# Performance work log

Hardware: AMD Instinct MI355X
Metric: run time of the kernel (lower is better)

The kernel has to match this reference:

```python
import jax, jax.numpy as jnp
import numpy as np

B, T, C = 4, 2048, 1024
H = 16
D = C // H  # head_dim = 64
SCALE = D ** -0.5


def setup_inputs() -> dict:
    key = jax.random.key(0)
    ks = jax.random.split(key, 5)
    x = jax.random.normal(ks[0], (B, T, C), dtype=jnp.float32)
    w_qkv = jax.random.normal(ks[1], (3 * C, C), dtype=jnp.float32) * (C ** -0.5)
    b_qkv = jnp.zeros((3 * C,), dtype=jnp.float32)
    w_proj = jax.random.normal(ks[2], (C, C), dtype=jnp.float32) * (C ** -0.5)
    b_proj = jnp.zeros((C,), dtype=jnp.float32)
    return {"x": x, "w_qkv": w_qkv, "b_qkv": b_qkv, "w_proj": w_proj, "b_proj": b_proj}


def reference(x, w_qkv, b_qkv, w_proj, b_proj):
    b, t, c = x.shape
    # fused qkv projection (torch Linear: x @ W.T + b)
    qkv = x @ w_qkv.T + b_qkv                      # [B, T, 3C]
    q, k, v = jnp.split(qkv, 3, axis=2)
    # [B, T, C] -> [B, H, T, D]
    q = q.reshape(b, t, H, D).transpose(0, 2, 1, 3)
    k = k.reshape(b, t, H, D).transpose(0, 2, 1, 3)
    v = v.reshape(b, t, H, D).transpose(0, 2, 1, 3)
    att = jnp.einsum('bhqd,bhkd->bhqk', q, k) * SCALE
    causal = jnp.tril(jnp.ones((t, t), dtype=bool))  # True = keep
    att = jnp.where(causal, att, -jnp.inf)
    att = jax.nn.softmax(att, axis=-1)
    out = jnp.einsum('bhqk,bhkd->bhqd', att, v)
    out = out.transpose(0, 2, 1, 3).reshape(b, t, c)
    return out @ w_proj.T + b_proj
```

## Files before the change

### kernel.cpp

```cpp
#include <hip/hip_runtime.h>

typedef unsigned short u16;
typedef __attribute__((ext_vector_type(8))) short short8;
typedef __attribute__((ext_vector_type(4))) float f32x4;
typedef __attribute__((ext_vector_type(16))) float f32x16;
typedef __attribute__((ext_vector_type(2))) unsigned uint2v;
typedef __attribute__((ext_vector_type(4))) unsigned u32x4;

#define AS1 __attribute__((address_space(1)))
#define AS3 __attribute__((address_space(3)))

constexpr int Bn = 4, Tn = 2048, Cn = 1024, Hn = 16, Dn = 64;
constexpr float SCL_LOG2E = 0.125f * 1.44269504088896f;

__device__ __forceinline__ u16 f2bf(float f) {
  union { float f; unsigned u; } v; v.f = f;
  unsigned r = v.u + 0x7FFFu + ((v.u >> 16) & 1u);
  return (u16)(r >> 16);
}

__device__ __forceinline__ unsigned cvtpk_bf16(float a, float b) {
  unsigned r;
  asm("v_cvt_pk_bf16_f32 %0, %1, %2" : "=v"(r) : "v"(a), "v"(b));
  return r;
}

__global__ void cast_all_bf16(const float* __restrict__ in0, u16* __restrict__ o0, int n0,
                              const float* __restrict__ in1, u16* __restrict__ o1, int n1,
                              const float* __restrict__ in2, u16* __restrict__ o2, int n2) {
  int i = blockIdx.x * 256 + threadIdx.x;
  const float* src;
  u16* dst;
  if (i < n0) { src = in0; dst = o0; }
  else if (i < n0 + n1) { i -= n0; src = in1; dst = o1; }
  else { i -= n0 + n1; if (i >= n2) return; src = in2; dst = o2; }
  float4 v = ((const float4*)src)[i];
  ushort4 o;
  o.x = f2bf(v.x); o.y = f2bf(v.y); o.z = f2bf(v.z); o.w = f2bf(v.w);
  ((ushort4*)dst)[i] = o;
}

template <typename OT>
__global__ __launch_bounds__(512) void gemm8(
    const u16* __restrict__ A, const u16* __restrict__ Bm,
    const float* __restrict__ bias, OT* __restrict__ C,
    int M, int N, int K, int nbn, int qcols, float qscale)
{
  __shared__ u16 As[2][128 * 64];
  __shared__ u16 Bs[2][128 * 64];

  const int tid = threadIdx.x;
  const int lane = tid & 63;
  const int w = tid >> 6;
  const int wm = w >> 2, wn = w & 3;
  const int l15 = lane & 15, lg = lane >> 4;

  const int nwg = gridDim.x;
  const int wg = (blockIdx.x & 7) * (nwg >> 3) + (blockIdx.x >> 3);
  const int m0 = (wg / nbn) * 128;
  const int n0 = (wg % nbn) * 128;
  const int NT = K >> 6;

  const int wrow = wm * 64;
  const int wcol = wn * 32;

  f32x4 acc[4][2] = {};

  auto stage_A = [&](int tt) {
    if (tt >= NT) return;
    const int bu = tt & 1;
#pragma unroll
    for (int it = 0; it < 2; ++it) {
      const int c = it * 512 + tid;
      const int row = c >> 3;
      const int cs = (c & 7) ^ (row & 7);
      const u16* g = A + (size_t)(m0 + row) * K + tt * 64 + cs * 8;
      __builtin_amdgcn_global_load_lds((const AS1 void*)g,
          (AS3 void*)(&As[bu][c * 8]), 16, 0, 0);
    }
  };
  auto stage_B = [&](int tt) {
    if (tt >= NT) return;
    const int bu = tt & 1;
#pragma unroll
    for (int it = 0; it < 2; ++it) {
      const int c = it * 512 + tid;
      const int row = c >> 3;
      const int cs = (c & 7) ^ (row & 7);
      const u16* g = Bm + (size_t)(n0 + row) * K + tt * 64 + cs * 8;
      __builtin_amdgcn_global_load_lds((const AS1 void*)g,
          (AS3 void*)(&Bs[bu][c * 8]), 16, 0, 0);
    }
  };

  auto readA = [&](int bu, int mh, short8 (*a)[2]) {
#pragma unroll
    for (int i = 0; i < 2; ++i)
#pragma unroll
      for (int ks = 0; ks < 2; ++ks) {
        const int ra = wrow + (mh * 2 + i) * 16 + l15;
        a[i][ks] = *(const short8*)(&As[bu][ra * 64 + (((ks * 4 + lg) ^ (ra & 7)) << 3)]);
      }
  };
  auto readB = [&](int bu, int nh, short8 (*b)[2]) {
#pragma unroll
    for (int ks = 0; ks < 2; ++ks) {
      const int rb = wcol + nh * 16 + l15;
      b[0][ks] = *(const short8*)(&Bs[bu][rb * 64 + (((ks * 4 + lg) ^ (rb & 7)) << 3)]);
    }
  };
  auto mmaq = [&](int mh, int nh, short8 (*a)[2], short8 (*b)[2]) {
    __builtin_amdgcn_s_setprio(1);
#pragma unroll
    for (int i = 0; i < 2; ++i)
#pragma unroll
      for (int ks = 0; ks < 2; ++ks)
        acc[mh * 2 + i][nh] = __builtin_amdgcn_mfma_f32_16x16x32_bf16(
            a[i][ks], b[0][ks], acc[mh * 2 + i][nh], 0, 0, 0);
    __builtin_amdgcn_s_setprio(0);
  };

  stage_A(0);
  stage_B(0);
  stage_A(1);
  asm volatile("s_waitcnt vmcnt(2)" ::: "memory");
  __builtin_amdgcn_sched_barrier(0);
  __builtin_amdgcn_s_barrier();

  for (int t = 0; t < NT; ++t) {
    const int bu = t & 1;
    short8 a0[2][2], a1[2][2], b0[1][2], b1[1][2];
    readA(bu, 0, a0);
    readB(bu, 0, b0);
    stage_B(t + 1);
    __builtin_amdgcn_s_barrier();
    mmaq(0, 0, a0, b0);
    __builtin_amdgcn_s_barrier();
    readB(bu, 1, b1);
    __builtin_amdgcn_s_barrier();
    mmaq(0, 1, a0, b1);
    __builtin_amdgcn_s_barrier();
    readA(bu, 1, a1);
    __builtin_amdgcn_s_barrier();
    mmaq(1, 1, a1, b1);
    __builtin_amdgcn_s_barrier();
    stage_A(t + 2);
    __builtin_amdgcn_s_barrier();
    mmaq(1, 0, a1, b0);
    if (t + 2 < NT) {
      asm volatile("s_waitcnt vmcnt(2)" ::: "memory");
      __builtin_amdgcn_sched_barrier(0);
    } else if (t + 1 < NT) {
      asm volatile("s_waitcnt vmcnt(0)" ::: "memory");
      __builtin_amdgcn_sched_barrier(0);
    }
    __builtin_amdgcn_s_barrier();
  }

  __syncthreads();
  if constexpr (__is_same(OT, u16)) {
    u16* bounce = &As[0][0];
#pragma unroll
    for (int i = 0; i < 4; ++i)
#pragma unroll
      for (int j = 0; j < 2; ++j) {
        const int colg = n0 + wcol + j * 16 + l15;
        const float sc = (colg < qcols) ? qscale : 1.0f;
        const float bv = bias[colg];
#pragma unroll
        for (int r = 0; r < 4; ++r)
          bounce[(wrow + i * 16 + lg * 4 + r) * 128 + wcol + j * 16 + l15] =
              f2bf((acc[i][j][r] + bv) * sc);
      }
    __syncthreads();
#pragma unroll
    for (int s = 0; s < 4; ++s) {
      const int u = s * 512 + tid;
      const int row = u >> 4, col = (u & 15) * 8;
      *(short8*)(C + (size_t)(m0 + row) * N + n0 + col) =
          *(const short8*)(&bounce[row * 128 + col]);
    }
  } else {
    float* bounce = (float*)&As[0][0];
#pragma unroll
    for (int cch = 0; cch < 2; ++cch) {
      if (wm == cch) {
#pragma unroll
        for (int i = 0; i < 4; ++i)
#pragma unroll
          for (int j = 0; j < 2; ++j) {
            const int colg = n0 + wcol + j * 16 + l15;
            const float bv = bias[colg];
#pragma unroll
            for (int r = 0; r < 4; ++r)
              bounce[(i * 16 + lg * 4 + r) * 128 + wcol + j * 16 + l15] =
                  acc[i][j][r] + bv;
          }
      }
      __syncthreads();
#pragma unroll
      for (int s = 0; s < 4; ++s) {
        const int u = s * 512 + tid;
        const int row = u >> 5, col = (u & 31) * 4;
        *(f32x4*)((float*)C + (size_t)(m0 + cch * 64 + row) * N + n0 + col) =
            *(const f32x4*)(&bounce[row * 128 + col]);
      }
      __syncthreads();
    }
  }
}

__global__ __launch_bounds__(256) void transpose_v(
    const u16* __restrict__ qkv, u16* __restrict__ vt)
{
  __shared__ u16 tile[64][72];
  const int bh = blockIdx.x >> 5;
  const int tt = blockIdx.x & 31;
  const int b = bh >> 4;
  const int h = bh & 15;
  const int tid = threadIdx.x;
  const int trow = tid >> 2;
  const int dseg = tid & 3;

  const u16* src = qkv + (size_t)(b * Tn + tt * 64 + trow) * (3 * Cn) + 2 * Cn + h * Dn + dseg * 16;
  short8 v0 = *(const short8*)src;
  short8 v1 = *(const short8*)(src + 8);
#pragma unroll
  for (int e = 0; e < 8; ++e) {
    tile[dseg * 16 + e][trow] = (u16)v0[e];
    tile[dseg * 16 + 8 + e][trow] = (u16)v1[e];
  }
  __syncthreads();

  const int drow = tid >> 2;
  const int tseg = tid & 3;
  u16* dst = vt + (size_t)(bh * Dn + drow) * Tn + tt * 64 + tseg * 16;
  *(short8*)dst = *(const short8*)&tile[drow][tseg * 16];
  *(short8*)(dst + 8) = *(const short8*)&tile[drow][tseg * 16 + 8];
}

__global__ __launch_bounds__(256) void attn_kernel(
    const u16* __restrict__ qkv, const u16* __restrict__ vt, u16* __restrict__ att)
{
  __shared__ u16 Ks[3][64 * 64];
  __shared__ u16 Vs[3][64 * 64];
  const int tid = threadIdx.x;
  const int lane = tid & 63;
  const int w = tid >> 6;
  const int l31 = lane & 31;
  const int hi = lane >> 5;

  const int blk = blockIdx.x;
  const int qt = (Tn / 128 - 1) - (blk >> 6);
  const int bh = blk & 63;
  const int b = bh >> 4;
  const int h = bh & 15;
  const int q0w = qt * 128 + w * 32;
  const int rowbase = b * Tn;
  const int koff = Cn + h * Dn;
  const size_t vbase = (size_t)bh * Dn * Tn;
  const int nt = 2 * qt + 2;
  const int ntw = 2 * qt + 1 + (w >> 1);

  short8 qf[4];
  {
    const u16* qp = qkv + (size_t)(rowbase + q0w + l31) * (3 * Cn) + h * Dn + hi * 8;
#pragma unroll
    for (int sub = 0; sub < 4; ++sub) qf[sub] = *(const short8*)(qp + sub * 16);
  }

  float l_r = 0.f;
  f32x16 oacc[2] = {};

#define STAGE(buf, t_)                                                            \
  {                                                                               \
    const int kt_ = (t_) * 64;                                                    \
    _Pragma("unroll")                                                             \
    for (int it = 0; it < 2; ++it) {                                              \
      int c = it * 256 + tid;                                                     \
      int row = c >> 3;                                                           \
      int cs = (c & 7) ^ (row & 7);                                               \
      const u16* gk = qkv + (size_t)(rowbase + kt_ + row) * (3 * Cn) + koff + cs * 8; \
      __builtin_amdgcn_global_load_lds((const AS1 void*)gk, (AS3 void*)(&Ks[buf][c * 8]), 16, 0, 0); \
      const u16* gv = vt + vbase + (size_t)row * Tn + kt_ + cs * 8;               \
      __builtin_amdgcn_global_load_lds((const AS1 void*)gv, (AS3 void*)(&Vs[buf][c * 8]), 16, 0, 0); \
    }                                                                             \
  }

  STAGE(0, 0);
  STAGE(1, 1);
  asm volatile("s_waitcnt vmcnt(4)" ::: "memory");
  __builtin_amdgcn_sched_barrier(0);
  __builtin_amdgcn_s_barrier();
  __builtin_amdgcn_sched_barrier(0);

  for (int t = 0; t < nt; ++t) {
    const int cur = t % 3;
    if (t + 2 < nt) STAGE((t + 2) % 3, t + 2);
    if (t < ntw) {
      const int kt = t * 64;
      const u16* Kb = Ks[cur];
      const u16* Vb = Vs[cur];

      f32x16 s0 = {}, s1 = {};
#pragma unroll
      for (int sub = 0; sub < 4; ++sub) {
        const int ch = sub * 2 + hi;
        const int r0 = l31;
        short8 kf0 = *(const short8*)(Kb + r0 * 64 + ((ch ^ (r0 & 7)) << 3));
        s0 = __builtin_amdgcn_mfma_f32_32x32x16_bf16(kf0, qf[sub], s0, 0, 0, 0);
        const int r1 = 32 + l31;
        short8 kf1 = *(const short8*)(Kb + r1 * 64 + ((ch ^ (r1 & 7)) << 3));
        s1 = __builtin_amdgcn_mfma_f32_32x32x16_bf16(kf1, qf[sub], s1, 0, 0, 0);
      }

      if (kt + 63 > q0w) {
        const int qa = q0w + l31;
#pragma unroll
        for (int r = 0; r < 16; ++r) {
          const int k0 = kt + ((r & 3) + 8 * (r >> 2)) + 4 * hi;
          if (k0 > qa) s0[r] = -1e30f;
          if (k0 + 32 > qa) s1[r] = -1e30f;
        }
      }

      float ts[16];
#pragma unroll
      for (int r = 0; r < 16; ++r) {
        s0[r] = __builtin_amdgcn_exp2f(s0[r]);
        s1[r] = __builtin_amdgcn_exp2f(s1[r]);
        ts[r] = s0[r] + s1[r];
      }
#pragma unroll
      for (int st = 8; st >= 1; st >>= 1)
#pragma unroll
        for (int r = 0; r < st; ++r) ts[r] += ts[r + st];
      float ps = ts[0];
      ps += __shfl_xor(ps, 32);
      l_r += ps;

      short8 pfr[4];
#pragma unroll
      for (int ks = 0; ks < 4; ++ks) {
        const f32x16& sv = (ks < 2) ? s0 : s1;
        const int base = (ks & 1) * 8;
        unsigned a0 = cvtpk_bf16(sv[base + 0], sv[base + 1]);
        unsigned a1 = cvtpk_bf16(sv[base + 2], sv[base + 3]);
        unsigned b0 = cvtpk_bf16(sv[base + 4], sv[base + 5]);
        unsigned b1 = cvtpk_bf16(sv[base + 6], sv[base + 7]);
        uint2v s_0 = __builtin_amdgcn_permlane32_swap(a0, b0, false, false);
        uint2v s_1 = __builtin_amdgcn_permlane32_swap(a1, b1, false, false);
        union { u32x4 u; short8 s; } cvt;
        cvt.u = (u32x4){s_0.x, s_1.x, s_0.y, s_1.y};
        pfr[ks] = cvt.s;
      }

#pragma unroll
      for (int j = 0; j < 2; ++j) {
        const int rv = j * 32 + l31;
        const int rsw = (rv & 7) << 3;
#pragma unroll
        for (int ks = 0; ks < 4; ++ks) {
          short8 vf = *(const short8*)(Vb + rv * 64 + (((ks * 2 + hi) << 3) ^ rsw));
          oacc[j] = __builtin_amdgcn_mfma_f32_32x32x16_bf16(vf, pfr[ks], oacc[j], 0, 0, 0);
        }
      }
    }
    if (t + 2 < nt)      asm volatile("s_waitcnt vmcnt(4)" ::: "memory");
    else if (t + 1 < nt) asm volatile("s_waitcnt vmcnt(0)" ::: "memory");
    __builtin_amdgcn_sched_barrier(0);
    __builtin_amdgcn_s_barrier();
    __builtin_amdgcn_sched_barrier(0);
  }

  {
    const float inv = __builtin_amdgcn_rcpf(l_r);
    u16* orow = att + (size_t)(rowbase + q0w + l31) * Cn + h * Dn + hi * 4;
#pragma unroll
    for (int j = 0; j < 2; ++j)
#pragma unroll
      for (int g = 0; g < 4; ++g) {
        ushort4 o;
#pragma unroll
        for (int c = 0; c < 4; ++c) o[c] = f2bf(oacc[j][g * 4 + c] * inv);
        *(ushort4*)(orow + j * 32 + g * 8) = o;
      }
  }
#undef STAGE
}

extern "C" void kernel_launch(void* const* d_in, const int* in_sizes, int n_in,
                              void* d_out, int out_size, void* d_ws, size_t ws_size,
                              hipStream_t stream) {
  const float* x      = (const float*)d_in[0];
  const float* w_qkv  = (const float*)d_in[1];
  const float* b_qkv  = (const float*)d_in[2];
  const float* w_proj = (const float*)d_in[3];
  const float* b_proj = (const float*)d_in[4];
  float* out = (float*)d_out;

  char* ws = (char*)d_ws;
  u16* x_bf     = (u16*)(ws);
  u16* wqkv_bf  = (u16*)(ws + 16777216);
  u16* wproj_bf = (u16*)(ws + 16777216 + 6291456);
  u16* qkv      = (u16*)(ws + 25165824);
  u16* att      = (u16*)(ws + 75497472);
  u16* vt       = x_bf;

  const int M = Bn * Tn;

  const int nq0 = M * Cn / 4, nq1 = 3 * Cn * Cn / 4, nq2 = Cn * Cn / 4;
  cast_all_bf16<<<(nq0 + nq1 + nq2 + 255) / 256, 256, 0, stream>>>(
      x, x_bf, nq0, w_qkv, wqkv_bf, nq1, w_proj, wproj_bf, nq2);

  gemm8<u16><<<1536, 512, 0, stream>>>(
      x_bf, wqkv_bf, b_qkv, qkv, M, 3 * Cn, Cn, 24, Cn, SCL_LOG2E);

  transpose_v<<<Bn * Hn * (Tn / 64), 256, 0, stream>>>(qkv, vt);

  attn_kernel<<<Bn * Hn * (Tn / 128), 256, 0, stream>>>(qkv, vt, att);

  gemm8<float><<<512, 512, 0, stream>>>(
      att, wproj_bf, b_proj, out, M, Cn, Cn, 8, 0, 1.0f);
}
```

Before: 170.7 us.

## Process 64 query rows per wave in attention to reuse K/V fragments

```diff
diff --git a/kernel.cpp b/kernel.cpp
--- a/kernel.cpp
+++ b/kernel.cpp
@@ -251,26 +251,27 @@
   const int hi = lane >> 5;
 
   const int blk = blockIdx.x;
-  const int qt = (Tn / 128 - 1) - (blk >> 6);
+  const int qt = 7 - (blk >> 6);
   const int bh = blk & 63;
   const int b = bh >> 4;
   const int h = bh & 15;
-  const int q0w = qt * 128 + w * 32;
+  const int q0w = qt * 256 + w * 64;
   const int rowbase = b * Tn;
   const int koff = Cn + h * Dn;
   const size_t vbase = (size_t)bh * Dn * Tn;
-  const int nt = 2 * qt + 2;
-  const int ntw = 2 * qt + 1 + (w >> 1);
-
-  short8 qf[4];
-  {
-    const u16* qp = qkv + (size_t)(rowbase + q0w + l31) * (3 * Cn) + h * Dn + hi * 8;
-#pragma unroll
-    for (int sub = 0; sub < 4; ++sub) qf[sub] = *(const short8*)(qp + sub * 16);
-  }
-
-  float l_r = 0.f;
-  f32x16 oacc[2] = {};
+  const int nt = 4 * qt + 4;
+  const int ntw = 4 * qt + w + 1;
+
+  short8 qf[2][4];
+#pragma unroll
+  for (int g = 0; g < 2; ++g) {
+    const u16* qp = qkv + (size_t)(rowbase + q0w + g * 32 + l31) * (3 * Cn) + h * Dn + hi * 8;
+#pragma unroll
+    for (int sub = 0; sub < 4; ++sub) qf[g][sub] = *(const short8*)(qp + sub * 16);
+  }
+
+  float l_r0 = 0.f, l_r1 = 0.f;
+  f32x16 oacc[2][2] = {};
 
 #define STAGE(buf, t_)                                                            \
   {                                                                               \
@@ -302,57 +303,65 @@
       const u16* Kb = Ks[cur];
       const u16* Vb = Vs[cur];
 
-      f32x16 s0 = {}, s1 = {};
+      f32x16 s0g0 = {}, s1g0 = {}, s0g1 = {}, s1g1 = {};
 #pragma unroll
       for (int sub = 0; sub < 4; ++sub) {
         const int ch = sub * 2 + hi;
         const int r0 = l31;
         short8 kf0 = *(const short8*)(Kb + r0 * 64 + ((ch ^ (r0 & 7)) << 3));
-        s0 = __builtin_amdgcn_mfma_f32_32x32x16_bf16(kf0, qf[sub], s0, 0, 0, 0);
         const int r1 = 32 + l31;
         short8 kf1 = *(const short8*)(Kb + r1 * 64 + ((ch ^ (r1 & 7)) << 3));
-        s1 = __builtin_amdgcn_mfma_f32_32x32x16_bf16(kf1, qf[sub], s1, 0, 0, 0);
-      }
-
-      if (kt + 63 > q0w) {
-        const int qa = q0w + l31;
+        s0g0 = __builtin_amdgcn_mfma_f32_32x32x16_bf16(kf0, qf[0][sub], s0g0, 0, 0, 0);
+        s1g0 = __builtin_amdgcn_mfma_f32_32x32x16_bf16(kf1, qf[0][sub], s1g0, 0, 0, 0);
+        s0g1 = __builtin_amdgcn_mfma_f32_32x32x16_bf16(kf0, qf[1][sub], s0g1, 0, 0, 0);
+        s1g1 = __builtin_amdgcn_mfma_f32_32x32x16_bf16(kf1, qf[1][sub], s1g1, 0, 0, 0);
+      }
+
+      short8 pfr0[4], pfr1[4];
+#pragma unroll
+      for (int g = 0; g < 2; ++g) {
+        f32x16& s0 = g ? s0g1 : s0g0;
+        f32x16& s1 = g ? s1g1 : s1g0;
+        const int qbase = q0w + g * 32;
+        if (kt + 63 > qbase) {
+          const int qa = qbase + l31;
+#pragma unroll
+          for (int r = 0; r < 16; ++r) {
+            const int k0 = kt + ((r & 3) + 8 * (r >> 2)) + 4 * hi;
+            if (k0 > qa) s0[r] = -1e30f;
+            if (k0 + 32 > qa) s1[r] = -1e30f;
+          }
+        }
+        float ts[16];
 #pragma unroll
         for (int r = 0; r < 16; ++r) {
-          const int k0 = kt + ((r & 3) + 8 * (r >> 2)) + 4 * hi;
-          if (k0 > qa) s0[r] = -1e30f;
-          if (k0 + 32 > qa) s1[r] = -1e30f;
+          s0[r] = __builtin_amdgcn_exp2f(s0[r]);
+          s1[r] = __builtin_amdgcn_exp2f(s1[r]);
+          ts[r] = s0[r] + s1[r];
         }
-      }
-
-      float ts[16];
-#pragma unroll
-      for (int r = 0; r < 16; ++r) {
-        s0[r] = __builtin_amdgcn_exp2f(s0[r]);
-        s1[r] = __builtin_amdgcn_exp2f(s1[r]);
-        ts[r] = s0[r] + s1[r];
-      }
-#pragma unroll
-      for (int st = 8; st >= 1; st >>= 1)
-#pragma unroll
-        for (int r = 0; r < st; ++r) ts[r] += ts[r + st];
-      float ps = ts[0];
-      ps += __shfl_xor(ps, 32);
-      l_r += ps;
-
-      short8 pfr[4];
-#pragma unroll
-      for (int ks = 0; ks < 4; ++ks) {
-        const f32x16& sv = (ks < 2) ? s0 : s1;
-        const int base = (ks & 1) * 8;
-        unsigned a0 = cvtpk_bf16(sv[base + 0], sv[base + 1]);
-        unsigned a1 = cvtpk_bf16(sv[base + 2], sv[base + 3]);
-        unsigned b0 = cvtpk_bf16(sv[base + 4], sv[base + 5]);
-        unsigned b1 = cvtpk_bf16(sv[base + 6], sv[base + 7]);
-        uint2v s_0 = __builtin_amdgcn_permlane32_swap(a0, b0, false, false);
-        uint2v s_1 = __builtin_amdgcn_permlane32_swap(a1, b1, false, false);
-        union { u32x4 u; short8 s; } cvt;
-        cvt.u = (u32x4){s_0.x, s_1.x, s_0.y, s_1.y};
-        pfr[ks] = cvt.s;
+#pragma unroll
+        for (int st = 8; st >= 1; st >>= 1)
+#pragma unroll
+          for (int r = 0; r < st; ++r) ts[r] += ts[r + st];
+        float ps = ts[0];
+        ps += __shfl_xor(ps, 32);
+        if (g) l_r1 += ps; else l_r0 += ps;
+
+        short8* pfr = g ? pfr1 : pfr0;
+#pragma unroll
+        for (int ks = 0; ks < 4; ++ks) {
+          const f32x16& sv = (ks < 2) ? s0 : s1;
+          const int base = (ks & 1) * 8;
+          unsigned a0 = cvtpk_bf16(sv[base + 0], sv[base + 1]);
+          unsigned a1 = cvtpk_bf16(sv[base + 2], sv[base + 3]);
+          unsigned b0 = cvtpk_bf16(sv[base + 4], sv[base + 5]);
+          unsigned b1 = cvtpk_bf16(sv[base + 6], sv[base + 7]);
+          uint2v s_0 = __builtin_amdgcn_permlane32_swap(a0, b0, false, false);
+          uint2v s_1 = __builtin_amdgcn_permlane32_swap(a1, b1, false, false);
+          union { u32x4 u; short8 s; } cvt;
+          cvt.u = (u32x4){s_0.x, s_1.x, s_0.y, s_1.y};
+          pfr[ks] = cvt.s;
+        }
       }
 
 #pragma unroll
@@ -362,7 +371,8 @@
 #pragma unroll
         for (int ks = 0; ks < 4; ++ks) {
           short8 vf = *(const short8*)(Vb + rv * 64 + (((ks * 2 + hi) << 3) ^ rsw));
-          oacc[j] = __builtin_amdgcn_mfma_f32_32x32x16_bf16(vf, pfr[ks], oacc[j], 0, 0, 0);
+          oacc[0][j] = __builtin_amdgcn_mfma_f32_32x32x16_bf16(vf, pfr0[ks], oacc[0][j], 0, 0, 0);
+          oacc[1][j] = __builtin_amdgcn_mfma_f32_32x32x16_bf16(vf, pfr1[ks], oacc[1][j], 0, 0, 0);
         }
       }
     }
@@ -373,17 +383,18 @@
     __builtin_amdgcn_sched_barrier(0);
   }
 
-  {
-    const float inv = __builtin_amdgcn_rcpf(l_r);
-    u16* orow = att + (size_t)(rowbase + q0w + l31) * Cn + h * Dn + hi * 4;
+#pragma unroll
+  for (int g = 0; g < 2; ++g) {
+    const float inv = __builtin_amdgcn_rcpf(g ? l_r1 : l_r0);
+    u16* orow = att + (size_t)(rowbase + q0w + g * 32 + l31) * Cn + h * Dn + hi * 4;
 #pragma unroll
     for (int j = 0; j < 2; ++j)
 #pragma unroll
-      for (int g = 0; g < 4; ++g) {
+      for (int gg = 0; gg < 4; ++gg) {
         ushort4 o;
 #pragma unroll
-        for (int c = 0; c < 4; ++c) o[c] = f2bf(oacc[j][g * 4 + c] * inv);
-        *(ushort4*)(orow + j * 32 + g * 8) = o;
+        for (int c = 0; c < 4; ++c) o[c] = f2bf(oacc[g][j][gg * 4 + c] * inv);
+        *(ushort4*)(orow + j * 32 + gg * 8) = o;
       }
   }
 #undef STAGE
@@ -418,7 +429,7 @@
 
   transpose_v<<<Bn * Hn * (Tn / 64), 256, 0, stream>>>(qkv, vt);
 
-  attn_kernel<<<Bn * Hn * (Tn / 128), 256, 0, stream>>>(qkv, vt, att);
+  attn_kernel<<<8 * 64, 256, 0, stream>>>(qkv, vt, att);
 
   gemm8<float><<<512, 512, 0, stream>>>(
       att, wproj_bf, b_proj, out, M, Cn, Cn, 8, 0, 1.0f);
```

New measurement: 196.2 us. +15.0%, slower.

## Fuse V transpose into QKV GEMM epilogue via swizzled LDS bounce

Applied to the files above, without the earlier changes.

```diff
diff --git a/kernel.cpp b/kernel.cpp
--- a/kernel.cpp
+++ b/kernel.cpp
@@ -44,6 +44,7 @@
 __global__ __launch_bounds__(512) void gemm8(
     const u16* __restrict__ A, const u16* __restrict__ Bm,
     const float* __restrict__ bias, OT* __restrict__ C,
+    u16* __restrict__ vtp,
     int M, int N, int K, int nbn, int qcols, float qscale)
 {
   __shared__ u16 As[2][128 * 64];
@@ -159,26 +160,57 @@
 
   __syncthreads();
   if constexpr (__is_same(OT, u16)) {
-    u16* bounce = &As[0][0];
-#pragma unroll
-    for (int i = 0; i < 4; ++i)
-#pragma unroll
-      for (int j = 0; j < 2; ++j) {
-        const int colg = n0 + wcol + j * 16 + l15;
-        const float sc = (colg < qcols) ? qscale : 1.0f;
-        const float bv = bias[colg];
-#pragma unroll
-        for (int r = 0; r < 4; ++r)
-          bounce[(wrow + i * 16 + lg * 4 + r) * 128 + wcol + j * 16 + l15] =
-              f2bf((acc[i][j][r] + bv) * sc);
-      }
-    __syncthreads();
-#pragma unroll
-    for (int s = 0; s < 4; ++s) {
-      const int u = s * 512 + tid;
-      const int row = u >> 4, col = (u & 15) * 8;
-      *(short8*)(C + (size_t)(m0 + row) * N + n0 + col) =
-          *(const short8*)(&bounce[row * 128 + col]);
+    if (vtp != nullptr && n0 >= 2 * Cn) {
+      u16* bt = &As[0][0];
+#pragma unroll
+      for (int i = 0; i < 4; ++i)
+#pragma unroll
+        for (int j = 0; j < 2; ++j) {
+          const int c = wcol + j * 16 + l15;
+          const float bv = bias[n0 + c];
+#pragma unroll
+          for (int r = 0; r < 4; ++r) {
+            const int rr = wrow + i * 16 + lg * 4 + r;
+            bt[c * 128 + (((rr >> 3) ^ (c & 15)) << 3) + (rr & 7)] =
+                f2bf(acc[i][j][r] + bv);
+          }
+        }
+      __syncthreads();
+      const int b = m0 >> 11;
+      const int t0 = m0 & 2047;
+      const int hbase = (n0 - 2 * Cn) >> 6;
+#pragma unroll
+      for (int s = 0; s < 4; ++s) {
+        const int u = s * 512 + tid;
+        const int c = u >> 4;
+        const int seg = u & 15;
+        short8 v = *(const short8*)(&bt[c * 128 + ((seg ^ (c & 15)) << 3)]);
+        const int head = hbase + (c >> 6);
+        const int dl = c & 63;
+        *(short8*)(vtp + (size_t)((b * Hn + head) * Dn + dl) * Tn + t0 + seg * 8) = v;
+      }
+    } else {
+      u16* bounce = &As[0][0];
+#pragma unroll
+      for (int i = 0; i < 4; ++i)
+#pragma unroll
+        for (int j = 0; j < 2; ++j) {
+          const int colg = n0 + wcol + j * 16 + l15;
+          const float sc = (colg < qcols) ? qscale : 1.0f;
+          const float bv = bias[colg];
+#pragma unroll
+          for (int r = 0; r < 4; ++r)
+            bounce[(wrow + i * 16 + lg * 4 + r) * 128 + wcol + j * 16 + l15] =
+                f2bf((acc[i][j][r] + bv) * sc);
+        }
+      __syncthreads();
+#pragma unroll
+      for (int s = 0; s < 4; ++s) {
+        const int u = s * 512 + tid;
+        const int row = u >> 4, col = (u & 15) * 8;
+        *(short8*)(C + (size_t)(m0 + row) * N + n0 + col) =
+            *(const short8*)(&bounce[row * 128 + col]);
+      }
     }
   } else {
     float* bounce = (float*)&As[0][0];
@@ -405,7 +437,9 @@
   u16* wproj_bf = (u16*)(ws + 16777216 + 6291456);
   u16* qkv      = (u16*)(ws + 25165824);
   u16* att      = (u16*)(ws + 75497472);
-  u16* vt       = x_bf;
+
+  const bool fuse = (ws_size >= 92274688u + 16777216u);
+  u16* vt = fuse ? (u16*)(ws + 92274688) : x_bf;
 
   const int M = Bn * Tn;
 
@@ -414,12 +448,14 @@
       x, x_bf, nq0, w_qkv, wqkv_bf, nq1, w_proj, wproj_bf, nq2);
 
   gemm8<u16><<<1536, 512, 0, stream>>>(
-      x_bf, wqkv_bf, b_qkv, qkv, M, 3 * Cn, Cn, 24, Cn, SCL_LOG2E);
-
-  transpose_v<<<Bn * Hn * (Tn / 64), 256, 0, stream>>>(qkv, vt);
+      x_bf, wqkv_bf, b_qkv, qkv, fuse ? vt : nullptr,
+      M, 3 * Cn, Cn, 24, Cn, SCL_LOG2E);
+
+  if (!fuse)
+    transpose_v<<<Bn * Hn * (Tn / 64), 256, 0, stream>>>(qkv, vt);
 
   attn_kernel<<<Bn * Hn * (Tn / 128), 256, 0, stream>>>(qkv, vt, att);
 
   gemm8<float><<<512, 512, 0, stream>>>(
-      att, wproj_bf, b_proj, out, M, Cn, Cn, 8, 0, 1.0f);
-}
+      att, wproj_bf, b_proj, out, nullptr, M, Cn, Cn, 8, 0, 1.0f);
+}
```

New measurement: 161.7 us, median of 2. 1.06x faster.
